# Kernel optimization log

Measured on AMD Instinct MI355X. Metric: run time of the kernel, lower is better.

The kernel has to match this reference:

```python
import jax, jax.numpy as jnp
import numpy as np
import math

N = 768; C_S = 384; C_Z = 128; H = 12; C = 16; P_QK = 4; P_V = 8; C_Z4 = C_Z // 4
INF = 1e5; EPS = 1e-8; LN_EPS = 1e-5


def setup_inputs() -> dict:
    key = jax.random.key(0)
    ks = jax.random.split(key, 16)
    w = lambda k, shp, sc=0.02: jax.random.normal(k, shp, jnp.float32) * sc
    s = jax.random.normal(ks[0], (N, C_S), jnp.float32)
    z = jax.random.normal(ks[1], (N, N, C_Z), jnp.float32)
    m = jax.random.normal(ks[2], (N, 3, 3), jnp.float32)
    q, r_ = jnp.linalg.qr(m)
    rot = q * jnp.sign(jnp.diagonal(r_, axis1=-2, axis2=-1))[:, None, :]  # orthonormal frames
    trans = jax.random.normal(ks[3], (N, 3), jnp.float32) * 10.0
    return {
        "s": s, "z": z, "rot": rot, "trans": trans,
        "s_mask": jnp.ones((N,), jnp.float32),
        "g_s": jnp.ones((C_S,), jnp.float32), "b_s": jnp.zeros((C_S,), jnp.float32),
        "g_z": jnp.ones((C_Z,), jnp.float32), "b_z": jnp.zeros((C_Z,), jnp.float32),
        "Wq": w(ks[4], (C_S, H * C)), "Wk": w(ks[5], (C_S, H * C)), "Wv": w(ks[6], (C_S, H * C)),
        "Wqp": w(ks[7], (C_S, H * P_QK * 3)), "Wkp": w(ks[8], (C_S, H * P_QK * 3)),
        "Wvp": w(ks[9], (C_S, H * P_V * 3)),
        "Wb": w(ks[10], (C_Z, H)), "Wdz": w(ks[11], (C_Z, C_Z4)),
        "head_weights": jnp.zeros((H,), jnp.float32),
        "Wout": w(ks[12], (H * C, C_S)), "Woutb": w(ks[13], (H * C_Z4, C_S)),
        "Woutpts": w(ks[14], (H * P_V * 4, C_S)),
        "rigids_to_res_idx": jnp.arange(N, dtype=jnp.int32),
    }


def _ipa(s, z, rot, trans, s_mask, g_s, b_s, g_z, b_z, Wq, Wk, Wv, Wqp, Wkp, Wvp,
         Wb, Wdz, head_weights, Wout, Woutb, Woutpts, idx):
    def ln(x, g, b):
        mu = jnp.mean(x, -1, keepdims=True)
        var = jnp.mean((x - mu) ** 2, -1, keepdims=True)
        return (x - mu) * jax.lax.rsqrt(var + LN_EPS) * g + b

    s = ln(s, g_s, b_s)
    z = ln(z, g_z, b_z)
    n = s.shape[0]
    q = (s @ Wq).reshape(n, H, C)
    k = (s @ Wk).reshape(n, H, C)
    v = (s @ Wv).reshape(n, H, C)

    def to_global(pts):  # r.apply: R x + t, per residue
        return jnp.einsum('nij,npj->npi', rot, pts) + trans[:, None, :]

    q_pts = to_global((s @ Wqp).reshape(n, H * P_QK, 3))
    k_pts = to_global((s @ Wkp).reshape(n, H * P_QK, 3))
    v_pts = to_global((s @ Wvp).reshape(n, H * P_V, 3))

    b = z @ Wb                      # [N, N, H] pair bias
    pair_z = z @ Wdz                # [N, N, C_Z4]
    mask2 = s_mask[:, None] * s_mask[None, :]
    z_bias = b + (INF * (mask2 - 1.0))[..., None]
    z_bias = z_bias[idx][:, idx]    # broadcast z over rigids via rigid->res index
    pair_g = pair_z[idx][:, idx]

    qp = q_pts.reshape(n, H, P_QK, 3)
    kp = k_pts.reshape(n, H, P_QK, 3)
    d2 = jnp.sum((qp[:, None] - kp[None, :]) ** 2, -1)  # [N, N, H, P_QK]
    hw = jax.nn.softplus(head_weights) * math.sqrt(1.0 / (3 * (P_QK * 9.0 / 2)))
    pt_att = -0.5 * jnp.sum(d2, -1) * hw                # [N, N, H]

    a = (jnp.einsum('ihc,jhc->ijh', q, k) * math.sqrt(1.0 / (3 * C))
         + math.sqrt(1.0 / 3) * z_bias + pt_att)
    a = jax.nn.softmax(a, axis=1)                       # softmax over keys j

    o = jnp.einsum('ijh,jhc->ihc', a, v).reshape(n, H * C)
    vp = v_pts.reshape(n, H, P_V, 3)
    o_pt = jnp.einsum('ijh,jhpx->ihpx', a, vp).reshape(n, H * P_V, 3)
    o_pair = jnp.einsum('ijh,ijc->ihc', a, pair_g).reshape(n, H * C_Z4)

    # r.invert_apply: R^T (x - t)
    o_pt = jnp.einsum('nji,npj->npi', rot, o_pt - trans[:, None, :])
    o_pt_norm = jnp.sqrt(jnp.sum(o_pt ** 2, -1) + EPS)  # [N, H*P_V]
    pts_feat = jnp.concatenate([o_pt.reshape(n, -1), o_pt_norm], -1)
    return o @ Wout + o_pair @ Woutb + pts_feat @ Woutpts


def reference(s, z, rot, trans, s_mask, g_s, b_s, g_z, b_z, Wq, Wk, Wv, Wqp, Wkp, Wvp,
              Wb, Wdz, head_weights, Wout, Woutb, Woutpts, rigids_to_res_idx):
    return _ipa(s, z, rot, trans, s_mask, g_s, b_s, g_z, b_z, Wq, Wk, Wv, Wqp, Wkp,
                Wvp, Wb, Wdz, head_weights, Wout, Woutb, Woutpts, rigids_to_res_idx)
```

## Files before the change

### kernel.cpp

```cpp
#include <hip/hip_runtime.h>
#include <hip/hip_bf16.h>

#define NN 768
#define NSQ (768*768)
#define CS 384
#define CZ 128
#define HH 12
#define INF_ 1e5f
#define EPS_ 1e-8f
#define LN_EPS_ 1e-5f

typedef __attribute__((ext_vector_type(8))) short short8;
typedef __attribute__((ext_vector_type(4))) short short4_t;
typedef __attribute__((ext_vector_type(4))) float floatx4;

constexpr size_t OFF_SLN  = 0;
constexpr size_t OFF_PROJ = OFF_SLN + (size_t)768*384;
constexpr size_t OFF_QPG  = OFF_PROJ + (size_t)768*1152;
constexpr size_t OFF_KPG  = OFF_QPG + (size_t)768*144;
constexpr size_t OFF_VPG  = OFF_KPG + (size_t)768*144;
constexpr size_t OFF_WTBF = OFF_VPG + (size_t)768*288;
constexpr size_t OFF_HW   = OFF_WTBF + 4096;
constexpr size_t OFF_BIAS = OFF_HW + 16;
constexpr size_t OFF_ATT  = OFF_BIAS + (size_t)NSQ*6;
constexpr size_t OFF_PZ   = OFF_ATT + (size_t)12*NSQ;
constexpr size_t OFF_OCAT = OFF_PZ + (size_t)NSQ*16;

__device__ __forceinline__ unsigned short f2bf(float f){
    unsigned int u = __float_as_uint(f);
    u = (u + 0x7fffu + ((u >> 16) & 1u)) >> 16;
    return (unsigned short)u;
}
__device__ __forceinline__ float bf2f(unsigned short u){
    return __uint_as_float((unsigned int)u << 16);
}

__global__ __launch_bounds__(256) void k_setup(const float* __restrict__ Wb, const float* __restrict__ Wdz,
                                               const float* __restrict__ hwin, float* __restrict__ ws,
                                               float* __restrict__ out){
    int b = blockIdx.x, t = threadIdx.x;
    if (b < 2880){ ws[OFF_OCAT + (size_t)b*256 + t] = 0.f; return; }
    b -= 2880;
    if (b < 1152){ out[(size_t)b*256 + t] = 0.f; return; }
    b -= 1152;
    if (b < 24){
        unsigned short* wt = (unsigned short*)(ws + OFF_WTBF);
        int o = b*2 + (t>>7), k = t & 127;
        float v = 0.f;
        if (o < HH) v = Wb[k*HH + o];
        else if (o < 44) v = Wdz[k*32 + (o - HH)];
        wt[o*128 + k] = f2bf(v);
        return;
    }
    b -= 24;
    if (b == 0 && t < HH){
        ws[OFF_HW + t] = log1pf(expf(hwin[t])) * sqrtf(1.0f/54.0f);
    }
}

__global__ __launch_bounds__(256) void k_proj(const float* __restrict__ s, const float* __restrict__ gs,
                                              const float* __restrict__ bs,
                                              const float* __restrict__ Wq, const float* __restrict__ Wk,
                                              const float* __restrict__ Wv, const float* __restrict__ Wqp,
                                              const float* __restrict__ Wkp, const float* __restrict__ Wvp,
                                              float* __restrict__ ws){
    __shared__ float slds[16][CS];
    __shared__ float stats[16][2];
    int rt = blockIdx.x, ct = blockIdx.y, t = threadIdx.x;
    for (int ix = t; ix < 16*CS; ix += 256){
        int r = ix / CS, c = ix % CS;
        slds[r][c] = s[(size_t)(rt*16 + r)*CS + c];
    }
    __syncthreads();
    int w = t >> 6, lane = t & 63;
    for (int r = w; r < 16; r += 4){
        float sum = 0.f, sq = 0.f;
        #pragma unroll
        for (int c0 = 0; c0 < CS; c0 += 64){
            float x = slds[r][c0 + lane];
            sum += x; sq += x*x;
        }
        #pragma unroll
        for (int off = 32; off; off >>= 1){
            sum += __shfl_xor(sum, off, 64);
            sq  += __shfl_xor(sq , off, 64);
        }
        if (lane == 0){
            float mu = sum * (1.0f/CS);
            float var = sq * (1.0f/CS) - mu*mu;
            stats[r][0] = mu;
            stats[r][1] = rsqrtf(var + LN_EPS_);
        }
    }
    __syncthreads();
    for (int ix = t; ix < 16*CS; ix += 256){
        int r = ix / CS, c = ix % CS;
        slds[r][c] = (slds[r][c] - stats[r][0]) * stats[r][1] * gs[c] + bs[c];
    }
    __syncthreads();
    int col = ct*128 + (t & 127);
    int rg = t >> 7;
    const float* wp; int stride;
    if      (col < 192){ wp = Wq  + col;       stride = 192; }
    else if (col < 384){ wp = Wk  + (col-192); stride = 192; }
    else if (col < 576){ wp = Wv  + (col-384); stride = 192; }
    else if (col < 720){ wp = Wqp + (col-576); stride = 144; }
    else if (col < 864){ wp = Wkp + (col-720); stride = 144; }
    else               { wp = Wvp + (col-864); stride = 288; }
    float acc[8] = {0,0,0,0,0,0,0,0};
    for (int k = 0; k < CS; k += 4){
        float w0 = wp[(size_t)k*stride];
        float w1 = wp[(size_t)(k+1)*stride];
        float w2 = wp[(size_t)(k+2)*stride];
        float w3 = wp[(size_t)(k+3)*stride];
        #pragma unroll
        for (int r = 0; r < 8; r++){
            floatx4 sv = *(const floatx4*)&slds[rg*8+r][k];
            acc[r] += sv[0]*w0 + sv[1]*w1 + sv[2]*w2 + sv[3]*w3;
        }
    }
    float* proj = ws + OFF_PROJ;
    for (int r = 0; r < 8; r++) proj[(size_t)(rt*16 + rg*8 + r)*1152 + col] = acc[r];
}

__global__ __launch_bounds__(192) void k_pts(const float* __restrict__ rot, const float* __restrict__ trans,
                                             float* __restrict__ ws){
    int i = blockIdx.x, p = threadIdx.x;
    const float* proj = ws + OFF_PROJ + (size_t)i*1152;
    const float* src; float* dst;
    if (p < 48)      { src = proj + 576 + p*3;       dst = ws + OFF_QPG + (size_t)i*144 + p*3; }
    else if (p < 96) { src = proj + 720 + (p-48)*3;  dst = ws + OFF_KPG + (size_t)i*144 + (p-48)*3; }
    else             { src = proj + 864 + (p-96)*3;  dst = ws + OFF_VPG + (size_t)i*288 + (p-96)*3; }
    float x = src[0], y = src[1], z = src[2];
    const float* R = rot + (size_t)i*9;
    const float* T = trans + (size_t)i*3;
    dst[0] = R[0]*x + R[1]*y + R[2]*z + T[0];
    dst[1] = R[3]*x + R[4]*y + R[5]*z + T[1];
    dst[2] = R[6]*x + R[7]*y + R[8]*z + T[2];
}

__global__ __launch_bounds__(256) void k_z(const float* __restrict__ z, const float* __restrict__ gz,
                                           const float* __restrict__ bz, float* __restrict__ ws){
    __shared__ unsigned short zlds[64][136];
    int t = threadIdx.x;
    int pb = blockIdx.x * 64;
    int lane32 = t & 31;
    int col = lane32 * 4;
    floatx4 g4 = *(const floatx4*)(gz + col);
    floatx4 b4 = *(const floatx4*)(bz + col);
    const float* zbase = z + (size_t)pb * 128;
    #pragma unroll
    for (int g = 0; g < 8; g++){
        int row = g*8 + (t >> 5);
        floatx4 v = *(const floatx4*)(zbase + (size_t)g*1024 + (size_t)t*4);
        float sum = v[0]+v[1]+v[2]+v[3];
        float sq  = v[0]*v[0]+v[1]*v[1]+v[2]*v[2]+v[3]*v[3];
        #pragma unroll
        for (int off = 1; off <= 16; off <<= 1){
            sum += __shfl_xor(sum, off, 64);
            sq  += __shfl_xor(sq , off, 64);
        }
        float mu = sum * (1.0f/128.0f);
        float rstd = rsqrtf(sq*(1.0f/128.0f) - mu*mu + LN_EPS_);
        short4_t sv;
        sv[0] = (short)f2bf((v[0]-mu)*rstd*g4[0] + b4[0]);
        sv[1] = (short)f2bf((v[1]-mu)*rstd*g4[1] + b4[1]);
        sv[2] = (short)f2bf((v[2]-mu)*rstd*g4[2] + b4[2]);
        sv[3] = (short)f2bf((v[3]-mu)*rstd*g4[3] + b4[3]);
        *(short4_t*)&zlds[row][col] = sv;
    }
    __syncthreads();
    const unsigned short* wt = (const unsigned short*)(ws + OFF_WTBF);
    int lane = t & 63, wv = t >> 6;
    int m = lane & 15, quad = lane >> 4;
    short8 bfrag[3][4];
    #pragma unroll
    for (int ot = 0; ot < 3; ot++)
        #pragma unroll
        for (int ks = 0; ks < 4; ks++){
            int o = ot*16 + m;
            bfrag[ot][ks] = *(const short8*)(wt + o*128 + ks*32 + quad*8);
        }
    floatx4 acc[3] = {{0.f,0.f,0.f,0.f},{0.f,0.f,0.f,0.f},{0.f,0.f,0.f,0.f}};
    int rbase = wv*16;
    #pragma unroll
    for (int ks = 0; ks < 4; ks++){
        short8 a = *(const short8*)&zlds[rbase + m][ks*32 + quad*8];
        acc[0] = __builtin_amdgcn_mfma_f32_16x16x32_bf16(a, bfrag[0][ks], acc[0], 0, 0, 0);
        acc[1] = __builtin_amdgcn_mfma_f32_16x16x32_bf16(a, bfrag[1][ks], acc[1], 0, 0, 0);
        acc[2] = __builtin_amdgcn_mfma_f32_16x16x32_bf16(a, bfrag[2][ks], acc[2], 0, 0, 0);
    }
    __syncthreads();
    unsigned short* stb = &zlds[0][0];
    unsigned short* stp = &zlds[0][0] + 64*12;
    #pragma unroll
    for (int ot = 0; ot < 3; ot++){
        int o = ot*16 + m;
        #pragma unroll
        for (int rg = 0; rg < 4; rg++){
            int rp = rbase + quad*4 + rg;
            float val = acc[ot][rg];
            if (o < HH)      stb[rp*12 + o] = f2bf(val);
            else if (o < 44) stp[rp*32 + (o - HH)] = f2bf(val);
        }
    }
    __syncthreads();
    unsigned short* bias16 = (unsigned short*)(ws + OFF_BIAS);
    unsigned int*   pz32   = (unsigned int*)((unsigned short*)(ws + OFF_PZ));
    for (int ix = t; ix < 12*32; ix += 256){
        int o = ix >> 5, u = ix & 31;
        unsigned int val = (unsigned int)stb[(u*2)*12 + o] | ((unsigned int)stb[(u*2+1)*12 + o] << 16);
        *(unsigned int*)(bias16 + (size_t)o*NSQ + pb + u*2) = val;
    }
    for (int ix = t; ix < 64*16; ix += 256){
        int rp = ix >> 4, u = ix & 15;
        unsigned int val = (unsigned int)stp[rp*32 + u*2] | ((unsigned int)stp[rp*32 + u*2+1] << 16);
        pz32[(size_t)(pb + rp)*16 + u] = val;
    }
}

__global__ __launch_bounds__(256) void k_logits(const float* __restrict__ smask, const int* __restrict__ idx,
                                                float* __restrict__ ws){
    __shared__ float qlds[8][336];
    __shared__ float klds[32][338];
    int it = blockIdx.x, jt = blockIdx.y, t = threadIdx.x;
    const float* proj = ws + OFF_PROJ;
    const float* qpg  = ws + OFF_QPG;
    const float* kpg  = ws + OFF_KPG;
    const float* hw   = ws + OFF_HW;
    const unsigned short* bias16 = (const unsigned short*)(ws + OFF_BIAS);
    float* att = ws + OFF_ATT;
    for (int ix = t; ix < 8*336; ix += 256){
        int r = ix / 336, c = ix % 336;
        int i = it*8 + r;
        qlds[r][c] = (c < 192) ? proj[(size_t)i*1152 + c] : qpg[(size_t)i*144 + (c - 192)];
    }
    for (int ix = t; ix < 32*336; ix += 256){
        int r = ix / 336, c = ix % 336;
        int j = jt*32 + r;
        klds[r][c] = (c < 192) ? proj[(size_t)j*1152 + 192 + c] : kpg[(size_t)j*144 + (c - 192)];
    }
    __syncthreads();
    int jl = t & 31, grp = t >> 5;
    int i = it*8 + grp, j = jt*32 + jl;
    int ires = idx[i], jres = idx[j];
    float mterm = INF_ * (smask[ires]*smask[jres] - 1.0f);
    const float S1 = 0.14433756729740643f;
    const float S2 = 0.57735026918962576f;
    for (int h = 0; h < HH; h++){
        floatx4 q0 = *(const floatx4*)&qlds[grp][h*16];
        floatx4 q1 = *(const floatx4*)&qlds[grp][h*16+4];
        floatx4 q2 = *(const floatx4*)&qlds[grp][h*16+8];
        floatx4 q3 = *(const floatx4*)&qlds[grp][h*16+12];
        const float* kr = &klds[jl][h*16];
        float2 k0 = *(const float2*)(kr+0),  k1 = *(const float2*)(kr+2);
        float2 k2 = *(const float2*)(kr+4),  k3 = *(const float2*)(kr+6);
        float2 k4 = *(const float2*)(kr+8),  k5 = *(const float2*)(kr+10);
        float2 k6 = *(const float2*)(kr+12), k7 = *(const float2*)(kr+14);
        float qk = q0[0]*k0.x+q0[1]*k0.y+q0[2]*k1.x+q0[3]*k1.y
                 + q1[0]*k2.x+q1[1]*k2.y+q1[2]*k3.x+q1[3]*k3.y
                 + q2[0]*k4.x+q2[1]*k4.y+q2[2]*k5.x+q2[3]*k5.y
                 + q3[0]*k6.x+q3[1]*k6.y+q3[2]*k7.x+q3[3]*k7.y;
        floatx4 qp0 = *(const floatx4*)&qlds[grp][192+h*12];
        floatx4 qp1 = *(const floatx4*)&qlds[grp][192+h*12+4];
        floatx4 qp2 = *(const floatx4*)&qlds[grp][192+h*12+8];
        const float* kp = &klds[jl][192+h*12];
        float2 p0 = *(const float2*)(kp+0), p1 = *(const float2*)(kp+2);
        float2 p2 = *(const float2*)(kp+4), p3 = *(const float2*)(kp+6);
        float2 p4 = *(const float2*)(kp+8), p5 = *(const float2*)(kp+10);
        float d0 = qp0[0]-p0.x, d1 = qp0[1]-p0.y, d2a = qp0[2]-p1.x, d3 = qp0[3]-p1.y;
        float d4 = qp1[0]-p2.x, d5 = qp1[1]-p2.y, d6 = qp1[2]-p3.x, d7 = qp1[3]-p3.y;
        float d8 = qp2[0]-p4.x, d9 = qp2[1]-p4.y, dA = qp2[2]-p5.x, dB = qp2[3]-p5.y;
        float d2 = d0*d0+d1*d1+d2a*d2a+d3*d3 + d4*d4+d5*d5+d6*d6+d7*d7 + d8*d8+d9*d9+dA*dA+dB*dB;
        float bv = bf2f(bias16[(size_t)h*NSQ + (size_t)ires*NN + jres]);
        float lg = qk*S1 + S2*(bv + mterm) - 0.5f*hw[h]*d2;
        att[(size_t)h*NSQ + (size_t)i*NN + j] = lg;
    }
}

__global__ __launch_bounds__(256) void k_softmax(float* __restrict__ ws){
    int t = threadIdx.x;
    int w = t >> 6, lane = t & 63;
    size_t rowi = (size_t)blockIdx.x*4 + w;
    float* row = ws + OFF_ATT + rowi*NN;
    floatx4 v0 = *(floatx4*)(row + lane*4);
    floatx4 v1 = *(floatx4*)(row + 256 + lane*4);
    floatx4 v2 = *(floatx4*)(row + 512 + lane*4);
    float mx = fmaxf(fmaxf(fmaxf(v0[0],v0[1]), fmaxf(v0[2],v0[3])),
               fmaxf(fmaxf(fmaxf(v1[0],v1[1]), fmaxf(v1[2],v1[3])),
                     fmaxf(fmaxf(v2[0],v2[1]), fmaxf(v2[2],v2[3]))));
    #pragma unroll
    for (int off = 32; off; off >>= 1) mx = fmaxf(mx, __shfl_xor(mx, off, 64));
    floatx4 e0, e1, e2;
    #pragma unroll
    for (int u = 0; u < 4; u++){ e0[u] = expf(v0[u]-mx); e1[u] = expf(v1[u]-mx); e2[u] = expf(v2[u]-mx); }
    float s = e0[0]+e0[1]+e0[2]+e0[3] + e1[0]+e1[1]+e1[2]+e1[3] + e2[0]+e2[1]+e2[2]+e2[3];
    #pragma unroll
    for (int off = 32; off; off >>= 1) s += __shfl_xor(s, off, 64);
    float inv = 1.0f / s;
    #pragma unroll
    for (int u = 0; u < 4; u++){ e0[u] *= inv; e1[u] *= inv; e2[u] *= inv; }
    *(floatx4*)(row + lane*4) = e0;
    *(floatx4*)(row + 256 + lane*4) = e1;
    *(floatx4*)(row + 512 + lane*4) = e2;
}

__global__ __launch_bounds__(256) void k_ov(float* __restrict__ ws){
    __shared__ float wlds[128][41];
    __shared__ float plds[32][128];
    int h = blockIdx.x, it = blockIdx.y, zs = blockIdx.z, t = threadIdx.x;
    const float* proj = ws + OFF_PROJ;
    const float* vpg  = ws + OFF_VPG;
    const float* att  = ws + OFF_ATT + (size_t)h*NSQ;
    int c = t & 63, isub = t >> 6;
    float acc[8] = {0,0,0,0,0,0,0,0};
    for (int jt = zs*2; jt < zs*2+2; jt++){
        __syncthreads();
        for (int ix = t; ix < 128*40; ix += 256){
            int jj = ix / 40, cc = ix % 40;
            int j = jt*128 + jj;
            wlds[jj][cc] = (cc < 16) ? proj[(size_t)j*1152 + 384 + h*16 + cc]
                                     : vpg[(size_t)j*288 + h*24 + (cc - 16)];
        }
        for (int ix = t; ix < 32*128; ix += 256){
            int rr = ix >> 7, jj = ix & 127;
            plds[rr][jj] = att[(size_t)(it*32 + rr)*NN + jt*128 + jj];
        }
        __syncthreads();
        if (c < 40){
            for (int jj = 0; jj < 128; jj += 4){
                float w0 = wlds[jj][c], w1 = wlds[jj+1][c], w2 = wlds[jj+2][c], w3 = wlds[jj+3][c];
                #pragma unroll
                for (int rr = 0; rr < 8; rr++){
                    floatx4 pv = *(floatx4*)&plds[isub*8+rr][jj];
                    acc[rr] += pv[0]*w0 + pv[1]*w1 + pv[2]*w2 + pv[3]*w3;
                }
            }
        }
    }
    if (c < 40){
        float* ocat = ws + OFF_OCAT;
        int col = (c < 16) ? (h*16 + c) : (576 + h*24 + (c - 16));
        for (int rr = 0; rr < 8; rr++){
            int i = it*32 + isub*8 + rr;
            atomicAdd(&ocat[(size_t)i*960 + col], acc[rr]);
        }
    }
}

__global__ __launch_bounds__(384) void k_opair(const int* __restrict__ idx, float* __restrict__ ws){
    __shared__ float plds[12][132];
    __shared__ float pzlds[128][33];
    int i = blockIdx.x, jt = blockIdx.y, t = threadIdx.x;
    int ires = idx[i];
    const unsigned int* pzg = (const unsigned int*)((const unsigned short*)(ws + OFF_PZ) + (size_t)ires*NN*32);
    const float* att = ws + OFF_ATT;
    for (int ix = t; ix < 12*128; ix += 384){
        int hh = ix >> 7, jj = ix & 127;
        plds[hh][jj] = att[(size_t)hh*NSQ + (size_t)i*NN + jt*128 + jj];
    }
    for (int ix = t; ix < 128*16; ix += 384){
        int jj = ix >> 4, cp = ix & 15;
        int jres = idx[jt*128 + jj];
        unsigned int u2 = pzg[(size_t)jres*16 + cp];
        pzlds[jj][cp*2]   = __uint_as_float(u2 << 16);
        pzlds[jj][cp*2+1] = __uint_as_float(u2 & 0xffff0000u);
    }
    __syncthreads();
    int h = t >> 5, c = t & 31;
    float acc = 0.f;
    #pragma unroll 4
    for (int j = 0; j < 128; j++)
        acc += plds[h][j] * pzlds[j][c];
    float* oc = ws + OFF_OCAT + (size_t)i*960 + 192;
    atomicAdd(&oc[h*32 + c], acc);
}

__global__ __launch_bounds__(96) void k_ptfin(const float* __restrict__ rot, const float* __restrict__ trans,
                                              float* __restrict__ ws){
    int i = blockIdx.x, p = threadIdx.x;
    float* base = ws + OFF_OCAT + (size_t)i*960;
    float* pt = base + 576 + p*3;
    float x = pt[0] - trans[i*3+0];
    float y = pt[1] - trans[i*3+1];
    float z = pt[2] - trans[i*3+2];
    const float* R = rot + (size_t)i*9;
    float lx = R[0]*x + R[3]*y + R[6]*z;
    float ly = R[1]*x + R[4]*y + R[7]*z;
    float lz = R[2]*x + R[5]*y + R[8]*z;
    pt[0] = lx; pt[1] = ly; pt[2] = lz;
    base[864 + p] = sqrtf(lx*lx + ly*ly + lz*lz + EPS_);
}

__global__ __launch_bounds__(256) void k_out(const float* __restrict__ Wout, const float* __restrict__ Woutb,
                                             const float* __restrict__ Woutp, float* __restrict__ ws,
                                             float* __restrict__ out){
    __shared__ float olds[32][244];
    int it = blockIdx.x, ct = blockIdx.y, kc = blockIdx.z, t = threadIdx.x;
    const float* ocat = ws + OFF_OCAT;
    for (int ix = t; ix < 32*240; ix += 256){
        int r = ix / 240, kk = ix % 240;
        olds[r][kk] = ocat[(size_t)(it*32 + r)*960 + kc*240 + kk];
    }
    __syncthreads();
    int cl = t & 63, ig = t >> 6;
    int c0 = ct*128 + cl, c1 = c0 + 64;
    float acc0[8], acc1[8];
    #pragma unroll
    for (int r=0;r<8;r++){ acc0[r]=0; acc1[r]=0; }
    for (int kk = 0; kk < 240; kk += 4){
        float w0[4], w1[4];
        #pragma unroll
        for (int u = 0; u < 4; u++){
            int k = kc*240 + kk + u;
            const float* wrow = (k < 192) ? (Wout  + (size_t)k*CS)
                              : (k < 576) ? (Woutb + (size_t)(k-192)*CS)
                                          : (Woutp + (size_t)(k-576)*CS);
            w0[u] = wrow[c0]; w1[u] = wrow[c1];
        }
        #pragma unroll
        for (int r = 0; r < 8; r++){
            floatx4 ov = *(const floatx4*)&olds[ig*8 + r][kk];
            acc0[r] += ov[0]*w0[0] + ov[1]*w0[1] + ov[2]*w0[2] + ov[3]*w0[3];
            acc1[r] += ov[0]*w1[0] + ov[1]*w1[1] + ov[2]*w1[2] + ov[3]*w1[3];
        }
    }
    for (int r = 0; r < 8; r++){
        int i = it*32 + ig*8 + r;
        atomicAdd(&out[(size_t)i*CS + c0], acc0[r]);
        atomicAdd(&out[(size_t)i*CS + c1], acc1[r]);
    }
}

extern "C" void kernel_launch(void* const* d_in, const int* in_sizes, int n_in,
                              void* d_out, int out_size, void* d_ws, size_t ws_size,
                              hipStream_t stream){
    const float* s     = (const float*)d_in[0];
    const float* z     = (const float*)d_in[1];
    const float* rot   = (const float*)d_in[2];
    const float* trans = (const float*)d_in[3];
    const float* smask = (const float*)d_in[4];
    const float* gs    = (const float*)d_in[5];
    const float* bs    = (const float*)d_in[6];
    const float* gz    = (const float*)d_in[7];
    const float* bz    = (const float*)d_in[8];
    const float* Wq    = (const float*)d_in[9];
    const float* Wk    = (const float*)d_in[10];
    const float* Wv    = (const float*)d_in[11];
    const float* Wqp   = (const float*)d_in[12];
    const float* Wkp   = (const float*)d_in[13];
    const float* Wvp   = (const float*)d_in[14];
    const float* Wb    = (const float*)d_in[15];
    const float* Wdz   = (const float*)d_in[16];
    const float* hwin  = (const float*)d_in[17];
    const float* Wout  = (const float*)d_in[18];
    const float* Woutb = (const float*)d_in[19];
    const float* Woutp = (const float*)d_in[20];
    const int*   idx   = (const int*)d_in[21];
    float* ws  = (float*)d_ws;
    float* out = (float*)d_out;

    k_setup  <<<4057, 256, 0, stream>>>(Wb, Wdz, hwin, ws, out);
    k_proj   <<<dim3(48, 9), 256, 0, stream>>>(s, gs, bs, Wq, Wk, Wv, Wqp, Wkp, Wvp, ws);
    k_pts    <<<768, 192, 0, stream>>>(rot, trans, ws);
    k_z      <<<9216, 256, 0, stream>>>(z, gz, bz, ws);
    k_logits <<<dim3(96, 24), 256, 0, stream>>>(smask, idx, ws);
    k_softmax<<<2304, 256, 0, stream>>>(ws);
    k_ov     <<<dim3(12, 24, 3), 256, 0, stream>>>(ws);
    k_opair  <<<dim3(768, 6), 384, 0, stream>>>(idx, ws);
    k_ptfin  <<<768, 96, 0, stream>>>(rot, trans, ws);
    k_out    <<<dim3(24, 3, 4), 256, 0, stream>>>(Wout, Woutb, Woutp, ws, out);
}
```

Baseline: 793.4 us.

## Compute attention logits as bf16 MFMA GEMM with split-precision point terms

Recasts the per-head QK dot product and the point-distance term as a single 64-wide bf16 matrix product. A new prep kernel builds packed A and B feature rows, including hi/lo bf16 splits of the query and key points for extra precision, plus a per-key norm constant. The logits kernel then runs MFMA 16x16x32 tiles per head and adds the bias, mask and norm terms in the epilogue. This replaces scalar FP32 FMA work with matrix cores at the cost of an extra launch, more workspace, and bf16 rounding error in the logits, which is mitigated only partly by the split terms.

```diff
diff --git a/kernel.cpp b/kernel.cpp
--- a/kernel.cpp
+++ b/kernel.cpp
@@ -25,6 +25,9 @@
 constexpr size_t OFF_ATT  = OFF_BIAS + (size_t)NSQ*6;
 constexpr size_t OFF_PZ   = OFF_ATT + (size_t)12*NSQ;
 constexpr size_t OFF_OCAT = OFF_PZ + (size_t)NSQ*16;
+constexpr size_t OFF_ABF  = OFF_OCAT + (size_t)768*960;
+constexpr size_t OFF_BBF  = OFF_ABF + 294912;
+constexpr size_t OFF_CJ   = OFF_BBF + 294912;
 
 __device__ __forceinline__ unsigned short f2bf(float f){
     unsigned int u = __float_as_uint(f);
@@ -139,6 +142,50 @@
     dst[2] = R[6]*x + R[7]*y + R[8]*z + T[2];
 }
 
+__global__ __launch_bounds__(256) void k_feat(float* __restrict__ ws){
+    int i = blockIdx.x, t = threadIdx.x;
+    const float* proj = ws + OFF_PROJ + (size_t)i*1152;
+    const float* qpg  = ws + OFF_QPG + (size_t)i*144;
+    const float* kpg  = ws + OFF_KPG + (size_t)i*144;
+    unsigned short* Abf = (unsigned short*)(ws + OFF_ABF);
+    unsigned short* Bbf = (unsigned short*)(ws + OFF_BBF);
+    const float S1 = 0.14433756729740643f;
+    for (int ix = t; ix < 12*64; ix += 256){
+        int h = ix >> 6, c = ix & 63;
+        float hwv = ws[OFF_HW + h];
+        unsigned short ab = 0, bb = 0;
+        if (c < 16){
+            ab = f2bf(proj[h*16 + c]);
+            bb = f2bf(S1 * proj[192 + h*16 + c]);
+        } else if (c < 28){
+            int d = c - 16;
+            ab = f2bf(qpg[h*12 + d]);
+            bb = f2bf(hwv * kpg[h*12 + d]);
+        } else if (c < 40){
+            int d = c - 28;
+            float qp = qpg[h*12 + d];
+            unsigned short hi = f2bf(qp);
+            ab = f2bf(qp - bf2f(hi));
+            bb = f2bf(hwv * kpg[h*12 + d]);
+        } else if (c < 52){
+            int d = c - 40;
+            ab = f2bf(qpg[h*12 + d]);
+            float x = hwv * kpg[h*12 + d];
+            unsigned short xh = f2bf(x);
+            bb = f2bf(x - bf2f(xh));
+        }
+        Abf[((size_t)h*768 + i)*64 + c] = ab;
+        Bbf[((size_t)h*768 + i)*64 + c] = bb;
+    }
+    if (t < 12){
+        float hwv = ws[OFF_HW + t];
+        float s2 = 0.f;
+        #pragma unroll
+        for (int d = 0; d < 12; d++){ float kp = kpg[t*12 + d]; s2 += kp*kp; }
+        ws[OFF_CJ + (size_t)t*768 + i] = -0.5f * hwv * s2;
+    }
+}
+
 __global__ __launch_bounds__(256) void k_z(const float* __restrict__ z, const float* __restrict__ gz,
                                            const float* __restrict__ bz, float* __restrict__ ws){
     __shared__ unsigned short zlds[64][136];
@@ -219,62 +266,71 @@
     }
 }
 
-__global__ __launch_bounds__(256) void k_logits(const float* __restrict__ smask, const int* __restrict__ idx,
-                                                float* __restrict__ ws){
-    __shared__ float qlds[8][336];
-    __shared__ float klds[32][338];
-    int it = blockIdx.x, jt = blockIdx.y, t = threadIdx.x;
-    const float* proj = ws + OFF_PROJ;
-    const float* qpg  = ws + OFF_QPG;
-    const float* kpg  = ws + OFF_KPG;
-    const float* hw   = ws + OFF_HW;
-    const unsigned short* bias16 = (const unsigned short*)(ws + OFF_BIAS);
-    float* att = ws + OFF_ATT;
-    for (int ix = t; ix < 8*336; ix += 256){
-        int r = ix / 336, c = ix % 336;
-        int i = it*8 + r;
-        qlds[r][c] = (c < 192) ? proj[(size_t)i*1152 + c] : qpg[(size_t)i*144 + (c - 192)];
-    }
-    for (int ix = t; ix < 32*336; ix += 256){
-        int r = ix / 336, c = ix % 336;
-        int j = jt*32 + r;
-        klds[r][c] = (c < 192) ? proj[(size_t)j*1152 + 192 + c] : kpg[(size_t)j*144 + (c - 192)];
-    }
-    __syncthreads();
-    int jl = t & 31, grp = t >> 5;
-    int i = it*8 + grp, j = jt*32 + jl;
-    int ires = idx[i], jres = idx[j];
-    float mterm = INF_ * (smask[ires]*smask[jres] - 1.0f);
-    const float S1 = 0.14433756729740643f;
+__global__ __launch_bounds__(256) void k_lg(const float* __restrict__ smask, const int* __restrict__ idx,
+                                            float* __restrict__ ws){
+    __shared__ unsigned short Al[64][64];
+    __shared__ unsigned short Bl[64][64];
+    __shared__ int   idJ[64];
+    __shared__ float sIv[64];
+    __shared__ float sjv[64];
+    __shared__ float cjv[64];
+    int it = blockIdx.x, jt = blockIdx.y, h = blockIdx.z, t = threadIdx.x;
+    const unsigned int* Ag = (const unsigned int*)((const unsigned short*)(ws + OFF_ABF) + ((size_t)h*768 + it*64)*64);
+    const unsigned int* Bg = (const unsigned int*)((const unsigned short*)(ws + OFF_BBF) + ((size_t)h*768 + jt*64)*64);
+    for (int ix = t; ix < 64*32; ix += 256){
+        int r = ix >> 5, u = ix & 31;
+        int gs = ((u >> 2) ^ (r & 7));
+        int us = (gs << 2) | (u & 3);
+        ((unsigned int*)&Al[r][0])[us] = Ag[ix];
+        ((unsigned int*)&Bl[r][0])[us] = Bg[ix];
+    }
+    if (t < 64){
+        int i = it*64 + t, j = jt*64 + t;
+        int ii = idx[i], jj = idx[j];
+        sIv[t] = smask[ii];
+        idJ[t] = jj;
+        sjv[t] = INF_ * 0.57735026918962576f * (smask[jj] - 1.0f);
+        cjv[t] = ws[OFF_CJ + (size_t)h*768 + j];
+    }
+    __syncthreads();
+    int lane = t & 63, w = t >> 6;
+    int m = lane & 15, quad = lane >> 4;
+    short8 af0, af1;
+    {
+        int r = w*16 + m;
+        int g0 = (quad) ^ (r & 7);
+        int g1 = (quad + 4) ^ (r & 7);
+        af0 = *(const short8*)&Al[r][g0*8];
+        af1 = *(const short8*)&Al[r][g1*8];
+    }
+    floatx4 acc[4] = {{0.f,0.f,0.f,0.f},{0.f,0.f,0.f,0.f},{0.f,0.f,0.f,0.f},{0.f,0.f,0.f,0.f}};
+    #pragma unroll
+    for (int nt = 0; nt < 4; nt++){
+        int r = nt*16 + m;
+        int g0 = (quad) ^ (r & 7);
+        int g1 = (quad + 4) ^ (r & 7);
+        short8 bf0 = *(const short8*)&Bl[r][g0*8];
+        short8 bf1 = *(const short8*)&Bl[r][g1*8];
+        acc[nt] = __builtin_amdgcn_mfma_f32_16x16x32_bf16(af0, bf0, acc[nt], 0, 0, 0);
+        acc[nt] = __builtin_amdgcn_mfma_f32_16x16x32_bf16(af1, bf1, acc[nt], 0, 0, 0);
+    }
+    const unsigned short* bias16 = (const unsigned short*)(ws + OFF_BIAS) + (size_t)h*NSQ;
+    float* att = ws + OFF_ATT + (size_t)h*NSQ;
     const float S2 = 0.57735026918962576f;
-    for (int h = 0; h < HH; h++){
-        floatx4 q0 = *(const floatx4*)&qlds[grp][h*16];
-        floatx4 q1 = *(const floatx4*)&qlds[grp][h*16+4];
-        floatx4 q2 = *(const floatx4*)&qlds[grp][h*16+8];
-        floatx4 q3 = *(const floatx4*)&qlds[grp][h*16+12];
-        const float* kr = &klds[jl][h*16];
-        float2 k0 = *(const float2*)(kr+0),  k1 = *(const float2*)(kr+2);
-        float2 k2 = *(const float2*)(kr+4),  k3 = *(const float2*)(kr+6);
-        float2 k4 = *(const float2*)(kr+8),  k5 = *(const float2*)(kr+10);
-        float2 k6 = *(const float2*)(kr+12), k7 = *(const float2*)(kr+14);
-        float qk = q0[0]*k0.x+q0[1]*k0.y+q0[2]*k1.x+q0[3]*k1.y
-                 + q1[0]*k2.x+q1[1]*k2.y+q1[2]*k3.x+q1[3]*k3.y
-                 + q2[0]*k4.x+q2[1]*k4.y+q2[2]*k5.x+q2[3]*k5.y
-                 + q3[0]*k6.x+q3[1]*k6.y+q3[2]*k7.x+q3[3]*k7.y;
-        floatx4 qp0 = *(const floatx4*)&qlds[grp][192+h*12];
-        floatx4 qp1 = *(const floatx4*)&qlds[grp][192+h*12+4];
-        floatx4 qp2 = *(const floatx4*)&qlds[grp][192+h*12+8];
-        const float* kp = &klds[jl][192+h*12];
-        float2 p0 = *(const float2*)(kp+0), p1 = *(const float2*)(kp+2);
-        float2 p2 = *(const float2*)(kp+4), p3 = *(const float2*)(kp+6);
-        float2 p4 = *(const float2*)(kp+8), p5 = *(const float2*)(kp+10);
-        float d0 = qp0[0]-p0.x, d1 = qp0[1]-p0.y, d2a = qp0[2]-p1.x, d3 = qp0[3]-p1.y;
-        float d4 = qp1[0]-p2.x, d5 = qp1[1]-p2.y, d6 = qp1[2]-p3.x, d7 = qp1[3]-p3.y;
-        float d8 = qp2[0]-p4.x, d9 = qp2[1]-p4.y, dA = qp2[2]-p5.x, dB = qp2[3]-p5.y;
-        float d2 = d0*d0+d1*d1+d2a*d2a+d3*d3 + d4*d4+d5*d5+d6*d6+d7*d7 + d8*d8+d9*d9+dA*dA+dB*dB;
-        float bv = bf2f(bias16[(size_t)h*NSQ + (size_t)ires*NN + jres]);
-        float lg = qk*S1 + S2*(bv + mterm) - 0.5f*hw[h]*d2;
-        att[(size_t)h*NSQ + (size_t)i*NN + j] = lg;
+    #pragma unroll
+    for (int rg = 0; rg < 4; rg++){
+        int il = w*16 + quad*4 + rg;
+        int i  = it*64 + il;
+        int ires = idx[i];
+        float si = sIv[il];
+        const unsigned short* brow = bias16 + (size_t)ires*NN;
+        float* arow = att + (size_t)i*NN + jt*64;
+        #pragma unroll
+        for (int nt = 0; nt < 4; nt++){
+            int jl = nt*16 + m;
+            float bv = bf2f(brow[idJ[jl]]);
+            arow[jl] = acc[nt][rg] + S2*bv + si*sjv[jl] + cjv[jl];
+        }
     }
 }
 
@@ -463,8 +519,9 @@
     k_setup  <<<4057, 256, 0, stream>>>(Wb, Wdz, hwin, ws, out);
     k_proj   <<<dim3(48, 9), 256, 0, stream>>>(s, gs, bs, Wq, Wk, Wv, Wqp, Wkp, Wvp, ws);
     k_pts    <<<768, 192, 0, stream>>>(rot, trans, ws);
+    k_feat   <<<768, 256, 0, stream>>>(ws);
     k_z      <<<9216, 256, 0, stream>>>(z, gz, bz, ws);
-    k_logits <<<dim3(96, 24), 256, 0, stream>>>(smask, idx, ws);
+    k_lg     <<<dim3(12, 12, 12), 256, 0, stream>>>(smask, idx, ws);
     k_softmax<<<2304, 256, 0, stream>>>(ws);
     k_ov     <<<dim3(12, 24, 3), 256, 0, stream>>>(ws);
     k_opair  <<<dim3(768, 6), 384, 0, stream>>>(idx, ws);
```

Result: faster. 693.5 us (-12.6%).
